# Performance work log

Measured on AMD Instinct MI355X. Metric: run time of the kernel, lower is better.

## Reference

```python
import jax, jax.numpy as jnp
import numpy as np

E, T, H, I = 8, 1024, 2048, 1408

def setup_inputs() -> dict:
    key = jax.random.key(0)
    k1, k2, k3, k4 = jax.random.split(key, 4)
    scale = 1.0 / np.sqrt(H)
    return {
        "x": jax.random.normal(k1, (E, T, H), dtype=jnp.float32),
        "gate_proj": jax.random.normal(k2, (E, H, I), dtype=jnp.float32) * scale,
        "up_proj": jax.random.normal(k3, (E, H, I), dtype=jnp.float32) * scale,
        "down_proj": jax.random.normal(k4, (E, I, H), dtype=jnp.float32) * (1.0 / np.sqrt(I)),
    }

def reference(x, gate_proj, up_proj, down_proj):
    # x: [E, T, H]; per-expert SwiGLU MLP via batched matmuls
    gate = jax.nn.silu(jnp.einsum('eth,ehi->eti', x, gate_proj))
    up = jnp.einsum('eth,ehi->eti', x, up_proj)
    return jnp.einsum('eti,eih->eth', gate * up, down_proj)
```

## Files before the change

kernel.cpp:

```cpp
#include <hip/hip_runtime.h>
#include <hip/hip_bf16.h>
#include <stdint.h>

#define NE 8
#define NT 1024
#define NH 2048
#define NI 1408
#define NI2 (2 * NI)

typedef __attribute__((ext_vector_type(8))) short          bf16x8;
typedef __attribute__((ext_vector_type(8))) unsigned short u16x8;
typedef __attribute__((ext_vector_type(4))) float          f32x4;

__device__ __forceinline__ unsigned short f2bf(float f) {
  union { float f; uint32_t u; } v; v.f = f;
  uint32_t u = v.u;
  return (unsigned short)((u + 0x7FFFu + ((u >> 16) & 1u)) >> 16);
}

__device__ __forceinline__ void gload_lds16(const void* g, void* l) {
  __builtin_amdgcn_global_load_lds(
      (const __attribute__((address_space(1))) uint32_t*)g,
      (__attribute__((address_space(3))) uint32_t*)l, 16, 0, 0);
}

#define WAITV0() asm volatile("s_waitcnt vmcnt(0)" ::: "memory")
#define BAR() do { __builtin_amdgcn_sched_barrier(0); \
                   __builtin_amdgcn_s_barrier();      \
                   __builtin_amdgcn_sched_barrier(0); } while (0)

__global__ __launch_bounds__(256) void cvt_bf16(const float* __restrict__ src,
                                                unsigned short* __restrict__ dst,
                                                int n8) {
  int i = blockIdx.x * blockDim.x + threadIdx.x;
  const int stride = gridDim.x * blockDim.x;
  for (; i < n8; i += stride) {
    const float4 f0 = ((const float4*)src)[i * 2];
    const float4 f1 = ((const float4*)src)[i * 2 + 1];
    u16x8 o;
    o[0] = f2bf(f0.x); o[1] = f2bf(f0.y); o[2] = f2bf(f0.z); o[3] = f2bf(f0.w);
    o[4] = f2bf(f1.x); o[5] = f2bf(f1.y); o[6] = f2bf(f1.z); o[7] = f2bf(f1.w);
    ((u16x8*)dst)[i] = o;
  }
}

__global__ __launch_bounds__(256) void transpose_cvt(
    const float* __restrict__ src, unsigned short* __restrict__ dst,
    int R, int C, long estride, int ilv, int radd) {
  __shared__ float tile[64][65];
  const int e  = blockIdx.z;
  const int c0 = blockIdx.x * 64;
  const int r0 = blockIdx.y * 64;
  const float* s = src + (size_t)e * R * C;
  unsigned short* d = dst + (size_t)e * estride;
  const int tid = threadIdx.x;
  const int tr  = tid >> 4;
  const int tc  = (tid & 15) * 4;
  #pragma unroll
  for (int it = 0; it < 4; ++it) {
    const int r = it * 16 + tr;
    float4 v = *(const float4*)(s + (size_t)(r0 + r) * C + c0 + tc);
    tile[r][tc + 0] = v.x; tile[r][tc + 1] = v.y;
    tile[r][tc + 2] = v.z; tile[r][tc + 3] = v.w;
  }
  __syncthreads();
  const int oc = tid >> 2;
  const int rb = (tid & 3) * 16;
  u16x8 o0, o1;
  #pragma unroll
  for (int j = 0; j < 8; ++j) {
    o0[j] = f2bf(tile[rb + j][oc]);
    o1[j] = f2bf(tile[rb + 8 + j][oc]);
  }
  const int c  = c0 + oc;
  const int ro = ilv ? ((((c >> 4) << 5) | (c & 15)) | radd) : c;
  unsigned short* dp = d + (size_t)ro * R + r0 + rb;
  *(u16x8*)dp       = o0;
  *(u16x8*)(dp + 8) = o1;
}

template <int NBY, int KDIM, int MODE>
__global__ __launch_bounds__(256, 4) void gemm_async(
    const unsigned short* __restrict__ Ag,
    const unsigned short* __restrict__ Bg,
    void* __restrict__ outp) {
  constexpr int KT    = KDIM / 32;
  constexpr int CHUNK = NBY * 8;

  __shared__ __align__(16) unsigned short As[2][128 * 32];
  __shared__ __align__(16) unsigned short Bs[2][128 * 32];

  const int flat = blockIdx.x;
  const int orig = (flat & 7) * CHUNK + (flat >> 3);
  const int e    = orig / CHUNK;
  const int r    = orig % CHUNK;
  const int by   = r >> 3;
  const int bx   = r & 7;

  const int bm  = bx * 128;
  const int bnn = by * 128;

  const int tid  = threadIdx.x;
  const int lane = tid & 63;
  const int w    = tid >> 6;
  const int wrm  = (w >> 1) * 64;
  const int wcn  = (w & 1) * 64;

  const unsigned short* Ae = Ag + (size_t)e * 1024 * KDIM;
  const unsigned short* Be = Bg + (size_t)e * (NBY * 128) * KDIM;

  const int l16 = lane >> 2;
  const int jx  = (lane & 3) ^ ((lane >> 3) & 3);
  const unsigned short* aA = Ae + (size_t)(bm  + w * 32 + l16) * KDIM + jx * 8;
  const unsigned short* aB = Be + (size_t)(bnn + w * 32 + l16) * KDIM + jx * 8;

  f32x4 acc[4][4];
  #pragma unroll
  for (int i = 0; i < 4; ++i)
    #pragma unroll
    for (int j = 0; j < 4; ++j) acc[i][j] = f32x4{0.f, 0.f, 0.f, 0.f};

  const int aoff = (lane & 15) * 64 +
                   (((lane >> 4) ^ (((lane & 15) >> 1) & 3)) * 16);

  auto STAGE = [&](unsigned short* Ad, unsigned short* Bd, int t) {
    const int kb = t * 32;
    #pragma unroll
    for (int q = 0; q < 2; ++q)
      gload_lds16(aA + (size_t)q * 16 * KDIM + kb, Ad + (w * 32 + q * 16) * 32);
    #pragma unroll
    for (int q = 0; q < 2; ++q)
      gload_lds16(aB + (size_t)q * 16 * KDIM + kb, Bd + (w * 32 + q * 16) * 32);
  };

  auto ITER = [&](int t, const unsigned short* Ac, const unsigned short* Bc,
                  unsigned short* An, unsigned short* Bn) {
    WAITV0();
    BAR();
    const char* Ab = (const char*)Ac + wrm * 64;
    const char* Bb = (const char*)Bc + wcn * 64;
    bf16x8 a[4], b[4];
    #pragma unroll
    for (int mi = 0; mi < 4; ++mi)
      a[mi] = *(const bf16x8*)(Ab + mi * 1024 + aoff);
    #pragma unroll
    for (int nj = 0; nj < 4; ++nj)
      b[nj] = *(const bf16x8*)(Bb + nj * 1024 + aoff);
    if (t + 1 < KT) STAGE(An, Bn, t + 1);
    #pragma unroll
    for (int mi = 0; mi < 4; ++mi)
      #pragma unroll
      for (int nj = 0; nj < 4; ++nj)
        acc[mi][nj] = __builtin_amdgcn_mfma_f32_16x16x32_bf16(
            a[mi], b[nj], acc[mi][nj], 0, 0, 0);
  };

  STAGE(As[0], Bs[0], 0);

  #pragma unroll 1
  for (int t = 0; t < KT; t += 2) {
    ITER(t,     As[0], Bs[0], As[1], Bs[1]);
    ITER(t + 1, As[1], Bs[1], As[0], Bs[0]);
  }

  const int crow = (lane >> 4) * 4;
  const int ccol = lane & 15;
  if constexpr (MODE == 0) {
    float* oe = (float*)outp + (size_t)e * 1024 * (NBY * 128);
    #pragma unroll
    for (int mi = 0; mi < 4; ++mi)
      #pragma unroll
      for (int nj = 0; nj < 4; ++nj)
        #pragma unroll
        for (int j = 0; j < 4; ++j) {
          const int row = bm + wrm + mi * 16 + crow + j;
          const int col = bnn + wcn + nj * 16 + ccol;
          oe[(size_t)row * (NBY * 128) + col] = acc[mi][nj][j];
        }
  } else {
    unsigned short* he = (unsigned short*)outp + (size_t)e * 1024 * (NBY * 64);
    const int hcb = by * 64 + (wcn >> 1);
    #pragma unroll
    for (int mi = 0; mi < 4; ++mi)
      #pragma unroll
      for (int p = 0; p < 2; ++p)
        #pragma unroll
        for (int j = 0; j < 4; ++j) {
          const float g = acc[mi][2 * p][j];
          const float u = acc[mi][2 * p + 1][j];
          const float sv = g / (1.0f + __expf(-g)) * u;
          const int row = bm + wrm + mi * 16 + crow + j;
          const int col = hcb + p * 16 + ccol;
          he[(size_t)row * (NBY * 64) + col] = f2bf(sv);
        }
  }
}

extern "C" void kernel_launch(void* const* d_in, const int* in_sizes, int n_in,
                              void* d_out, int out_size, void* d_ws, size_t ws_size,
                              hipStream_t stream) {
  const float* x    = (const float*)d_in[0];
  const float* gate = (const float*)d_in[1];
  const float* up   = (const float*)d_in[2];
  const float* down = (const float*)d_in[3];
  float* out = (float*)d_out;

  unsigned short* x_bf = (unsigned short*)d_ws;
  unsigned short* wcat = x_bf + (size_t)NE * NT * NH;
  unsigned short* dT   = wcat + (size_t)NE * NI2 * NH;
  unsigned short* hb   = dT   + (size_t)NE * NH * NI;

  cvt_bf16<<<2048, 256, 0, stream>>>(x, x_bf, NE * NT * NH / 8);

  transpose_cvt<<<dim3(NI / 64, NH / 64, NE), 256, 0, stream>>>(
      gate, wcat, NH, NI, (long)NI2 * NH, 1, 0);
  transpose_cvt<<<dim3(NI / 64, NH / 64, NE), 256, 0, stream>>>(
      up, wcat, NH, NI, (long)NI2 * NH, 1, 16);
  transpose_cvt<<<dim3(NH / 64, NI / 64, NE), 256, 0, stream>>>(
      down, dT, NI, NH, (long)NH * NI, 0, 0);

  gemm_async<22, NH, 1><<<NE * 22 * 8, 256, 0, stream>>>(x_bf, wcat, hb);
  gemm_async<16, NI, 0><<<NE * 16 * 8, 256, 0, stream>>>(hb, dT, out);
}
```

Measured before the change: 286.9 us.

## Pre-swizzle operands into MFMA fragment layout and load directly into registers

The conversion and transpose kernels now write bf16 operands in a tiled layout that matches the MFMA 16x16x32 fragment order, so each lane's 16-byte load is its exact operand. The GEMM drops LDS staging and barriers entirely, register double-buffers global loads, and grows the block tile to 128x256 with each wave owning 128x64 (acc[8][4]). Occupancy drops to 2 blocks per CU and grid size halves. Each wave rereads the full A tile from global/L2 with no LDS sharing, which raises cache traffic and register pressure.

```diff
diff --git a/kernel.cpp b/kernel.cpp
--- a/kernel.cpp
+++ b/kernel.cpp
@@ -18,35 +18,32 @@
   return (unsigned short)((u + 0x7FFFu + ((u >> 16) & 1u)) >> 16);
 }
 
-__device__ __forceinline__ void gload_lds16(const void* g, void* l) {
-  __builtin_amdgcn_global_load_lds(
-      (const __attribute__((address_space(1))) uint32_t*)g,
-      (__attribute__((address_space(3))) uint32_t*)l, 16, 0, 0);
-}
-
-#define WAITV0() asm volatile("s_waitcnt vmcnt(0)" ::: "memory")
-#define BAR() do { __builtin_amdgcn_sched_barrier(0); \
-                   __builtin_amdgcn_s_barrier();      \
-                   __builtin_amdgcn_sched_barrier(0); } while (0)
-
-__global__ __launch_bounds__(256) void cvt_bf16(const float* __restrict__ src,
-                                                unsigned short* __restrict__ dst,
-                                                int n8) {
+
+__global__ __launch_bounds__(256) void cvt_frag(const float* __restrict__ src,
+                                                unsigned short* __restrict__ dst) {
+  const int n8 = NE * NT * NH / 8;
   int i = blockIdx.x * blockDim.x + threadIdx.x;
   const int stride = gridDim.x * blockDim.x;
   for (; i < n8; i += stride) {
+    const int k8 = i & (NH / 8 - 1);
+    const int t  = (i >> 8) & (NT - 1);
+    const int e  = i >> 18;
     const float4 f0 = ((const float4*)src)[i * 2];
     const float4 f1 = ((const float4*)src)[i * 2 + 1];
     u16x8 o;
     o[0] = f2bf(f0.x); o[1] = f2bf(f0.y); o[2] = f2bf(f0.z); o[3] = f2bf(f0.w);
     o[4] = f2bf(f1.x); o[5] = f2bf(f1.y); o[6] = f2bf(f1.z); o[7] = f2bf(f1.w);
-    ((u16x8*)dst)[i] = o;
-  }
-}
-
-__global__ __launch_bounds__(256) void transpose_cvt(
+    const int kt = k8 >> 2;
+    const int kb = k8 & 3;
+    const size_t off = (((size_t)e * (NH / 32) + kt) * (NT / 16) + (t >> 4)) * 512
+                     + kb * 128 + (t & 15) * 8;
+    *(u16x8*)(dst + off) = o;
+  }
+}
+
+__global__ __launch_bounds__(256) void transpose_frag(
     const float* __restrict__ src, unsigned short* __restrict__ dst,
-    int R, int C, long estride, int ilv, int radd) {
+    int R, int C, int CT16, long estride, int ilv, int radd) {
   __shared__ float tile[64][65];
   const int e  = blockIdx.z;
   const int c0 = blockIdx.x * 64;
@@ -74,125 +71,112 @@
   }
   const int c  = c0 + oc;
   const int ro = ilv ? ((((c >> 4) << 5) | (c & 15)) | radd) : c;
-  unsigned short* dp = d + (size_t)ro * R + r0 + rb;
-  *(u16x8*)dp       = o0;
-  *(u16x8*)(dp + 8) = o1;
+  const int k0 = r0 + rb;
+  const size_t off = (((size_t)(k0 >> 5)) * CT16 + (ro >> 4)) * 512
+                   + ((k0 & 31) >> 3) * 128 + (ro & 15) * 8;
+  *(u16x8*)(d + off)       = o0;
+  *(u16x8*)(d + off + 128) = o1;
 }
 
 template <int NBY, int KDIM, int MODE>
-__global__ __launch_bounds__(256, 4) void gemm_async(
+__global__ __launch_bounds__(256, 2) void gemm_frag(
     const unsigned short* __restrict__ Ag,
     const unsigned short* __restrict__ Bg,
     void* __restrict__ outp) {
   constexpr int KT    = KDIM / 32;
+  constexpr int AT    = NT / 16;
+  constexpr int BT    = NBY * 16;
   constexpr int CHUNK = NBY * 8;
-
-  __shared__ __align__(16) unsigned short As[2][128 * 32];
-  __shared__ __align__(16) unsigned short Bs[2][128 * 32];
 
   const int flat = blockIdx.x;
   const int orig = (flat & 7) * CHUNK + (flat >> 3);
   const int e    = orig / CHUNK;
   const int r    = orig % CHUNK;
+  const int bx   = r & 7;
   const int by   = r >> 3;
-  const int bx   = r & 7;
 
   const int bm  = bx * 128;
-  const int bnn = by * 128;
 
   const int tid  = threadIdx.x;
   const int lane = tid & 63;
   const int w    = tid >> 6;
-  const int wrm  = (w >> 1) * 64;
-  const int wcn  = (w & 1) * 64;
-
-  const unsigned short* Ae = Ag + (size_t)e * 1024 * KDIM;
-  const unsigned short* Be = Bg + (size_t)e * (NBY * 128) * KDIM;
-
-  const int l16 = lane >> 2;
-  const int jx  = (lane & 3) ^ ((lane >> 3) & 3);
-  const unsigned short* aA = Ae + (size_t)(bm  + w * 32 + l16) * KDIM + jx * 8;
-  const unsigned short* aB = Be + (size_t)(bnn + w * 32 + l16) * KDIM + jx * 8;
-
-  f32x4 acc[4][4];
+
+  const unsigned short* pa =
+      Ag + ((size_t)e * KT * AT + (bm >> 4)) * 512 + lane * 8;
+  const unsigned short* pb =
+      Bg + ((size_t)e * KT * BT + by * 16 + w * 4) * 512 + lane * 8;
+
+  f32x4 acc[8][4];
   #pragma unroll
-  for (int i = 0; i < 4; ++i)
+  for (int i = 0; i < 8; ++i)
     #pragma unroll
     for (int j = 0; j < 4; ++j) acc[i][j] = f32x4{0.f, 0.f, 0.f, 0.f};
 
-  const int aoff = (lane & 15) * 64 +
-                   (((lane >> 4) ^ (((lane & 15) >> 1) & 3)) * 16);
-
-  auto STAGE = [&](unsigned short* Ad, unsigned short* Bd, int t) {
-    const int kb = t * 32;
-    #pragma unroll
-    for (int q = 0; q < 2; ++q)
-      gload_lds16(aA + (size_t)q * 16 * KDIM + kb, Ad + (w * 32 + q * 16) * 32);
-    #pragma unroll
-    for (int q = 0; q < 2; ++q)
-      gload_lds16(aB + (size_t)q * 16 * KDIM + kb, Bd + (w * 32 + q * 16) * 32);
+  bf16x8 aE[8], bE[4], aO[8], bO[4];
+
+  auto LD = [&](bf16x8 (&a)[8], bf16x8 (&b)[4], int t) {
+    const bf16x8* A0 = (const bf16x8*)(pa + (size_t)t * AT * 512);
+    const bf16x8* B0 = (const bf16x8*)(pb + (size_t)t * BT * 512);
+    #pragma unroll
+    for (int mi = 0; mi < 8; ++mi) a[mi] = A0[mi * 64];
+    #pragma unroll
+    for (int nj = 0; nj < 4; ++nj) b[nj] = B0[nj * 64];
   };
-
-  auto ITER = [&](int t, const unsigned short* Ac, const unsigned short* Bc,
-                  unsigned short* An, unsigned short* Bn) {
-    WAITV0();
-    BAR();
-    const char* Ab = (const char*)Ac + wrm * 64;
-    const char* Bb = (const char*)Bc + wcn * 64;
-    bf16x8 a[4], b[4];
-    #pragma unroll
-    for (int mi = 0; mi < 4; ++mi)
-      a[mi] = *(const bf16x8*)(Ab + mi * 1024 + aoff);
-    #pragma unroll
-    for (int nj = 0; nj < 4; ++nj)
-      b[nj] = *(const bf16x8*)(Bb + nj * 1024 + aoff);
-    if (t + 1 < KT) STAGE(An, Bn, t + 1);
-    #pragma unroll
-    for (int mi = 0; mi < 4; ++mi)
+  auto FMA = [&](bf16x8 (&a)[8], bf16x8 (&b)[4]) {
+    #pragma unroll
+    for (int mi = 0; mi < 8; ++mi)
       #pragma unroll
       for (int nj = 0; nj < 4; ++nj)
         acc[mi][nj] = __builtin_amdgcn_mfma_f32_16x16x32_bf16(
             a[mi], b[nj], acc[mi][nj], 0, 0, 0);
   };
 
-  STAGE(As[0], Bs[0], 0);
-
+  LD(aE, bE, 0);
+  int t = 0;
   #pragma unroll 1
-  for (int t = 0; t < KT; t += 2) {
-    ITER(t,     As[0], Bs[0], As[1], Bs[1]);
-    ITER(t + 1, As[1], Bs[1], As[0], Bs[0]);
-  }
+  for (; t + 2 < KT; t += 2) {
+    LD(aO, bO, t + 1);
+    FMA(aE, bE);
+    LD(aE, bE, t + 2);
+    FMA(aO, bO);
+  }
+  LD(aO, bO, t + 1);
+  FMA(aE, bE);
+  FMA(aO, bO);
 
   const int crow = (lane >> 4) * 4;
   const int ccol = lane & 15;
   if constexpr (MODE == 0) {
-    float* oe = (float*)outp + (size_t)e * 1024 * (NBY * 128);
-    #pragma unroll
-    for (int mi = 0; mi < 4; ++mi)
+    float* oe = (float*)outp + (size_t)e * NT * (NBY * 256);
+    #pragma unroll
+    for (int mi = 0; mi < 8; ++mi)
       #pragma unroll
       for (int nj = 0; nj < 4; ++nj)
         #pragma unroll
         for (int j = 0; j < 4; ++j) {
-          const int row = bm + wrm + mi * 16 + crow + j;
-          const int col = bnn + wcn + nj * 16 + ccol;
-          oe[(size_t)row * (NBY * 128) + col] = acc[mi][nj][j];
+          const int row = bm + mi * 16 + crow + j;
+          const int col = by * 256 + w * 64 + nj * 16 + ccol;
+          oe[(size_t)row * (NBY * 256) + col] = acc[mi][nj][j];
         }
   } else {
-    unsigned short* he = (unsigned short*)outp + (size_t)e * 1024 * (NBY * 64);
-    const int hcb = by * 64 + (wcn >> 1);
-    #pragma unroll
-    for (int mi = 0; mi < 4; ++mi)
+    unsigned short* he = (unsigned short*)outp + (size_t)e * (NI / 32) * (NT / 16) * 512;
+    const int itile = by * 4 + w;
+    #pragma unroll
+    for (int mi = 0; mi < 8; ++mi)
       #pragma unroll
-      for (int p = 0; p < 2; ++p)
+      for (int p = 0; p < 2; ++p) {
+        const int kb = p * 2 + (ccol >> 3);
+        const int ic = ccol & 7;
+        const size_t base = ((size_t)itile * (NT / 16) + ((bm >> 4) + mi)) * 512
+                          + kb * 128 + (crow) * 8 + ic;
         #pragma unroll
         for (int j = 0; j < 4; ++j) {
           const float g = acc[mi][2 * p][j];
           const float u = acc[mi][2 * p + 1][j];
           const float sv = g / (1.0f + __expf(-g)) * u;
-          const int row = bm + wrm + mi * 16 + crow + j;
-          const int col = hcb + p * 16 + ccol;
-          he[(size_t)row * (NBY * 64) + col] = f2bf(sv);
+          he[base + j * 8] = f2bf(sv);
         }
+      }
   }
 }
 
@@ -210,15 +194,15 @@
   unsigned short* dT   = wcat + (size_t)NE * NI2 * NH;
   unsigned short* hb   = dT   + (size_t)NE * NH * NI;
 
-  cvt_bf16<<<2048, 256, 0, stream>>>(x, x_bf, NE * NT * NH / 8);
-
-  transpose_cvt<<<dim3(NI / 64, NH / 64, NE), 256, 0, stream>>>(
-      gate, wcat, NH, NI, (long)NI2 * NH, 1, 0);
-  transpose_cvt<<<dim3(NI / 64, NH / 64, NE), 256, 0, stream>>>(
-      up, wcat, NH, NI, (long)NI2 * NH, 1, 16);
-  transpose_cvt<<<dim3(NH / 64, NI / 64, NE), 256, 0, stream>>>(
-      down, dT, NI, NH, (long)NH * NI, 0, 0);
-
-  gemm_async<22, NH, 1><<<NE * 22 * 8, 256, 0, stream>>>(x_bf, wcat, hb);
-  gemm_async<16, NI, 0><<<NE * 16 * 8, 256, 0, stream>>>(hb, dT, out);
-}
+  cvt_frag<<<2048, 256, 0, stream>>>(x, x_bf);
+
+  transpose_frag<<<dim3(NI / 64, NH / 64, NE), 256, 0, stream>>>(
+      gate, wcat, NH, NI, NI2 / 16, (long)NI2 * NH, 1, 0);
+  transpose_frag<<<dim3(NI / 64, NH / 64, NE), 256, 0, stream>>>(
+      up, wcat, NH, NI, NI2 / 16, (long)NI2 * NH, 1, 16);
+  transpose_frag<<<dim3(NH / 64, NI / 64, NE), 256, 0, stream>>>(
+      down, dT, NI, NH, NH / 16, (long)NH * NI, 0, 0);
+
+  gemm_frag<11, NH, 1><<<NE * 11 * 8, 256, 0, stream>>>(x_bf, wcat, hb);
+  gemm_frag<8, NI, 0><<<NE * 8 * 8, 256, 0, stream>>>(hb, dT, out);
+}
```

Result: slower. 352.1 us (+22.8%).
